# Performance work log

Measured on AMD Instinct MI355X. Metric: run time of the kernel, lower is better.

Reference implementation:

```python
import jax, jax.numpy as jnp
import numpy as np

B, CIN, COUT = 16, 64, 64
H, W = 96, 96
HK, AK = 3, 3  # hidden_kernels, attn_kernels


def setup_inputs() -> dict:
    key = jax.random.key(0)
    k1, k2, k3, k4, k5 = jax.random.split(key, 5)
    s = 1.0 / np.sqrt(CIN * HK * HK)
    return {
        "x1": jax.random.normal(k1, (B, CIN, H, W), jnp.float32),
        "x2": jax.random.normal(k2, (B, CIN, H, W), jnp.float32),
        "w1": jax.random.normal(k3, (COUT, CIN, HK, HK), jnp.float32) * s,
        "w2": jax.random.normal(k4, (COUT, CIN, HK, HK), jnp.float32) * s,
        "w3": jax.random.normal(k5, (COUT, CIN, HK, HK), jnp.float32) * s,
    }


def _conv(x, w):
    p = HK // 2
    return jax.lax.conv_general_dilated(x, w, (1, 1), [(p, p), (p, p)])


def _unfold_strided(x):
    # nn.Unfold(AK, stride=AK): non-overlapping AK x AK patches.
    # [B,C,H,W] -> [B, C*AK*AK, (H//AK)*(W//AK)], channel order (C, kh, kw).
    b, c, h, w = x.shape
    hp, wp = h // AK, w // AK
    x = x.reshape(b, c, hp, AK, wp, AK).transpose(0, 1, 3, 5, 2, 4)
    return x.reshape(b, c * AK * AK, hp * wp)


def _unfold_padded(x):
    # nn.Unfold(AK, padding=AK//2): stride-1 patches, output length H*W (AK odd).
    b, c, h, w = x.shape
    p = AK // 2
    xp = jnp.pad(x, ((0, 0), (0, 0), (p, p), (p, p)))
    cols = [xp[:, :, i:i + h, j:j + w] for i in range(AK) for j in range(AK)]
    return jnp.stack(cols, axis=2).reshape(b, c * AK * AK, h * w)


def reference(x1, x2, w1, w2, w3):
    aa = AK * AK
    L = (H // AK) * (W // AK)
    kf = _conv(x1, w1)   # [B, Cout, H, W]
    qf = _conv(x2, w2)
    vf = _conv(x1, w3)
    # key: [B, aa, Cout, L]; query: [B, aa, L, Cout]
    key = _unfold_strided(kf).reshape(B, COUT, aa, L).transpose(0, 2, 1, 3)
    qry = _unfold_strided(qf).reshape(B, COUT, aa, L).transpose(0, 2, 3, 1)
    # scores[b,k,c,d] over patches -> [B, aa, Cout_k, Cout_q]
    scores = jnp.einsum('bkcl,bkld->bkcd', key, qry)
    # transpose(1,3).flatten(2): [B, Cout_q, Cout_k*aa]
    scores = scores.transpose(0, 3, 2, 1).reshape(B, COUT, COUT * aa)
    scores = scores / np.sqrt(COUT * aa).astype(np.float32)
    attn = jax.nn.softmax(scores, axis=2)  # dynamic conv kernels
    vcols = _unfold_padded(vf)             # [B, Cout*aa, H*W]
    out = jnp.einsum('bce,bel->bcl', attn, vcols)
    return out.reshape(B, COUT, H, W)
```

## Files before the change

### kernel.cpp

```cpp
#include <hip/hip_runtime.h>


typedef __attribute__((ext_vector_type(8))) short short8v;
typedef __attribute__((ext_vector_type(4))) float floatx4;
typedef __attribute__((ext_vector_type(4))) unsigned int uint4v;

constexpr int PLANE = 9216;
constexpr int SCP_STRIDE = 589824;

__device__ __forceinline__ unsigned short f2bf(float f) {
    unsigned int u = __float_as_uint(f);
    u = (u + 0x7FFFu + ((u >> 16) & 1u)) >> 16;
    return (unsigned short)u;
}

__global__ __launch_bounds__(256) void nchw2nhwc_bf16(
    const float* __restrict__ x, unsigned short* __restrict__ xh)
{
    int blk = blockIdx.x;
    int b = blk / 96, y = blk - b * 96;
    __shared__ float ls[64][96];
    const float* xp = x + (size_t)b * 64 * PLANE + (size_t)y * 96;
    for (int i = threadIdx.x; i < 64 * 96; i += 256) {
        int ci = i / 96, xc = i - ci * 96;
        ls[ci][xc] = xp[(size_t)ci * PLANE + xc];
    }
    __syncthreads();
    unsigned short* op = xh + ((size_t)b * PLANE + (size_t)y * 96) * 64;
    for (int i = threadIdx.x; i < 96 * 8; i += 256) {
        int xc = i >> 3, cg = i & 7;
        unsigned short tmp[8] __attribute__((aligned(16)));
        #pragma unroll
        for (int j = 0; j < 8; ++j) tmp[j] = f2bf(ls[cg * 8 + j][xc]);
        *(uint4v*)&op[(size_t)xc * 64 + cg * 8] = *(const uint4v*)tmp;
    }
}

__global__ __launch_bounds__(256) void wreorder(
    const float* __restrict__ w1, const float* __restrict__ w2,
    const float* __restrict__ w3, unsigned short* __restrict__ wl)
{
    int blk = blockIdx.x;
    int wi = blk / 9, k9 = blk - wi * 9;
    const float* w = (wi == 0) ? w1 : ((wi == 1) ? w2 : w3);
    unsigned short* o = wl + (size_t)wi * 9 * 4096 + (size_t)k9 * 4096;
    for (int i = threadIdx.x; i < 4096; i += 256)
        o[i] = f2bf(w[(size_t)i * 9 + k9]);
}

__global__ __launch_bounds__(256) void conv_mfma(
    const unsigned short* __restrict__ xh,
    const unsigned short* __restrict__ wl,
    void* __restrict__ out, int omode, int dynb)
{
    int blk = blockIdx.x;
    int xs3 = blk % 3; int t = blk / 3;
    int yq = t % 12;   int b = t / 12;
    int x0 = xs3 * 32, y0 = yq * 8;

    __shared__ __align__(16) unsigned short xs[10 * 34 * 64];

    const unsigned short* xb = xh + (size_t)b * PLANE * 64;
    for (int i = threadIdx.x; i < 2720; i += 256) {
        int g = i & 7, pix = i >> 3;
        int pr = pix / 34, pc = pix - pr * 34;
        int y = y0 - 1 + pr, x = x0 - 1 + pc;
        uint4v v = {0u, 0u, 0u, 0u};
        if ((unsigned)y < 96u && (unsigned)x < 96u)
            v = *(const uint4v*)&xb[((size_t)y * 96 + x) * 64 + g * 8];
        *(uint4v*)&xs[pix * 64 + (g ^ (pc & 7)) * 8] = v;
    }
    __syncthreads();

    int lane = threadIdx.x & 63;
    int w = threadIdx.x >> 6;
    int ln = lane & 15, quad = lane >> 4;
    int coh  = (w & 1) * 32;
    int rowh = (w >> 1) * 4;

    const unsigned short* wb = wl + (dynb ? (size_t)b * 9 * 4096 : 0);

    floatx4 acc[2][8];
    #pragma unroll
    for (int mi = 0; mi < 2; ++mi)
        #pragma unroll
        for (int nt = 0; nt < 8; ++nt) acc[mi][nt] = (floatx4){0.f, 0.f, 0.f, 0.f};

    #pragma unroll
    for (int k9 = 0; k9 < 9; ++k9) {
        int dy = k9 / 3, dx = k9 - dy * 3;
        #pragma unroll
        for (int ch = 0; ch < 2; ++ch) {
            short8v a0 = *(const short8v*)
                &wb[((size_t)k9 * 64 + coh + ln) * 64 + ch * 32 + quad * 8];
            short8v a1 = *(const short8v*)
                &wb[((size_t)k9 * 64 + coh + 16 + ln) * 64 + ch * 32 + quad * 8];
            int gb = ch * 4 + quad;
            #pragma unroll
            for (int nt = 0; nt < 8; ++nt) {
                int n = nt * 16 + ln;
                int r = rowh + (n >> 5) + dy;
                int c = (n & 31) + dx;
                short8v bf = *(const short8v*)
                    &xs[(r * 34 + c) * 64 + (gb ^ (c & 7)) * 8];
                acc[0][nt] = __builtin_amdgcn_mfma_f32_16x16x32_bf16(a0, bf, acc[0][nt], 0, 0, 0);
                acc[1][nt] = __builtin_amdgcn_mfma_f32_16x16x32_bf16(a1, bf, acc[1][nt], 0, 0, 0);
            }
        }
    }

    #pragma unroll
    for (int nt = 0; nt < 8; ++nt) {
        int n = nt * 16 + ln;
        int y = y0 + rowh + (n >> 5), x = x0 + (n & 31);
        if (omode == 2) {
            float* o = (float*)out;
            #pragma unroll
            for (int mi = 0; mi < 2; ++mi)
                #pragma unroll
                for (int reg = 0; reg < 4; ++reg) {
                    int co = coh + mi * 16 + quad * 4 + reg;
                    o[((size_t)(b * 64 + co)) * PLANE + (size_t)y * 96 + x] = acc[mi][nt][reg];
                }
        } else if (omode == 1) {
            unsigned short* o = (unsigned short*)out;
            #pragma unroll
            for (int mi = 0; mi < 2; ++mi) {
                unsigned short tmp[4] __attribute__((aligned(8)));
                #pragma unroll
                for (int reg = 0; reg < 4; ++reg) tmp[reg] = f2bf(acc[mi][nt][reg]);
                *(uint2*)&o[((size_t)b * PLANE + (size_t)y * 96 + x) * 64 + coh + mi * 16 + quad * 4]
                    = *(const uint2*)tmp;
            }
        } else {
            unsigned short* o = (unsigned short*)out;
            int k9 = (y % 3) * 3 + (x % 3);
            int l = (y / 3) * 32 + (x / 3);
            #pragma unroll
            for (int mi = 0; mi < 2; ++mi)
                #pragma unroll
                for (int reg = 0; reg < 4; ++reg) {
                    int co = coh + mi * 16 + quad * 4 + reg;
                    o[((size_t)(b * 9 + k9) * 64 + co) * 1024 + l] = f2bf(acc[mi][nt][reg]);
                }
        }
    }
}

__global__ __launch_bounds__(256) void scores_mfma(
    const unsigned short* __restrict__ kfc, const unsigned short* __restrict__ qfc,
    float* __restrict__ scp, int nseg)
{
    int blk = blockIdx.x;
    int seg = blk % nseg;
    int bk  = blk / nseg;
    int lane = threadIdx.x & 63, w = threadIdx.x >> 6;
    int ln = lane & 15, quad = lane >> 4;
    const unsigned short* ka = kfc + (size_t)bk * 64 * 1024;
    const unsigned short* qa = qfc + (size_t)bk * 64 * 1024;

    int Kblk = 1024 / nseg;
    int Kw   = Kblk / 4;
    int nch  = Kw / 32;

    floatx4 acc[4][4];
    #pragma unroll
    for (int i = 0; i < 4; ++i)
        #pragma unroll
        for (int j = 0; j < 4; ++j) acc[i][j] = (floatx4){0.f, 0.f, 0.f, 0.f};

    for (int chk = 0; chk < nch; ++chk) {
        int l = seg * Kblk + w * Kw + chk * 32 + quad * 8;
        short8v a[4], bq[4];
        #pragma unroll
        for (int mi = 0; mi < 4; ++mi)
            a[mi] = *(const short8v*)&ka[(size_t)(mi * 16 + ln) * 1024 + l];
        #pragma unroll
        for (int ni = 0; ni < 4; ++ni)
            bq[ni] = *(const short8v*)&qa[(size_t)(ni * 16 + ln) * 1024 + l];
        #pragma unroll
        for (int mi = 0; mi < 4; ++mi)
            #pragma unroll
            for (int ni = 0; ni < 4; ++ni)
                acc[mi][ni] = __builtin_amdgcn_mfma_f32_16x16x32_bf16(a[mi], bq[ni], acc[mi][ni], 0, 0, 0);
    }

    __shared__ float ls[4][64][65];
    #pragma unroll
    for (int mi = 0; mi < 4; ++mi)
        #pragma unroll
        for (int ni = 0; ni < 4; ++ni)
            #pragma unroll
            for (int reg = 0; reg < 4; ++reg)
                ls[w][ni * 16 + ln][mi * 16 + quad * 4 + reg] = acc[mi][ni][reg];
    __syncthreads();

    float* op = scp + (size_t)seg * SCP_STRIDE + (size_t)bk * 4096;
    int t = threadIdx.x;
    #pragma unroll
    for (int j = 0; j < 16; ++j) {
        int e = t * 16 + j;
        int d = e >> 6, c = e & 63;
        op[e] = ls[0][d][c] + ls[1][d][c] + ls[2][d][c] + ls[3][d][c];
    }
}

__global__ __launch_bounds__(256) void softmax_kernel(
    const float* __restrict__ scp, unsigned short* __restrict__ dynw, int nseg)
{
    int w = threadIdx.x >> 6, c = threadIdx.x & 63;
    int row = blockIdx.x * 4 + w;
    int b = row >> 6, d = row & 63;
    float v[9];
    float mx = -3.0e38f;
    #pragma unroll
    for (int k = 0; k < 9; ++k) {
        size_t idx = (size_t)(b * 9 + k) * 4096 + d * 64 + c;
        float s = scp[idx];
        for (int g = 1; g < nseg; ++g) s += scp[(size_t)g * SCP_STRIDE + idx];
        v[k] = s * (1.0f / 24.0f);
        mx = fmaxf(mx, v[k]);
    }
    #pragma unroll
    for (int o = 32; o; o >>= 1) mx = fmaxf(mx, __shfl_xor(mx, o));
    float sum = 0.f;
    #pragma unroll
    for (int k = 0; k < 9; ++k) { v[k] = __expf(v[k] - mx); sum += v[k]; }
    #pragma unroll
    for (int o = 32; o; o >>= 1) sum += __shfl_xor(sum, o);
    float inv = 1.0f / sum;
    #pragma unroll
    for (int k = 0; k < 9; ++k)
        dynw[((size_t)(b * 9 + k) * 64 + d) * 64 + c] = f2bf(v[k] * inv);
}

extern "C" void kernel_launch(void* const* d_in, const int* in_sizes, int n_in,
                              void* d_out, int out_size, void* d_ws, size_t ws_size,
                              hipStream_t stream) {
    (void)in_sizes; (void)n_in; (void)out_size;
    const float* x1 = (const float*)d_in[0];
    const float* x2 = (const float*)d_in[1];
    const float* w1 = (const float*)d_in[2];
    const float* w2 = (const float*)d_in[3];
    const float* w3 = (const float*)d_in[4];
    float* out = (float*)d_out;

    char* ws = (char*)d_ws;
    constexpr size_t XHB = (size_t)16 * PLANE * 64 * 2;
    unsigned short* xh1 = (unsigned short*)(ws);
    unsigned short* xh2 = (unsigned short*)(ws + XHB);
    unsigned short* kfc = (unsigned short*)(ws + 2 * XHB);
    unsigned short* qfc = (unsigned short*)(ws + 3 * XHB);
    unsigned short* wl  = (unsigned short*)(ws + 4 * XHB);
    unsigned short* dynw = (unsigned short*)(ws + 4 * XHB + 221184);
    float* scp = (float*)(ws + 4 * XHB + 221184 + 1179648);

    size_t base = 4 * XHB + 221184 + 1179648;
    int nseg = (ws_size >= base + 2 * (size_t)SCP_STRIDE * 4) ? 2 : 1;

    nchw2nhwc_bf16<<<dim3(1536), dim3(256), 0, stream>>>(x1, xh1);
    nchw2nhwc_bf16<<<dim3(1536), dim3(256), 0, stream>>>(x2, xh2);
    wreorder<<<dim3(27), dim3(256), 0, stream>>>(w1, w2, w3, wl);

    conv_mfma<<<dim3(576), dim3(256), 0, stream>>>(xh1, wl,            kfc, 3, 0);
    conv_mfma<<<dim3(576), dim3(256), 0, stream>>>(xh2, wl + 9 * 4096, qfc, 3, 0);
    scores_mfma<<<dim3(144 * nseg), dim3(256), 0, stream>>>(kfc, qfc, scp, nseg);
    softmax_kernel<<<dim3(256), dim3(256), 0, stream>>>(scp, dynw, nseg);
    conv_mfma<<<dim3(576), dim3(256), 0, stream>>>(xh1, wl + 18 * 4096, xh2, 1, 0);
    conv_mfma<<<dim3(576), dim3(256), 0, stream>>>(xh2, dynw, out, 2, 1);
}
```

Before: 286.9 us.

## Batch the three convolutions into one launch and retile conv per wave row

Merges the two NCHW->NHWC conversions into one launch. Fuses the k, q and v convolutions into a single conv_mfma grid of 3456 blocks, which writes v to a separate workspace buffer when the workspace is large enough. The conv tile shrinks from 8 rows to 4: each wave now owns one image row and computes all 64 output channels, loading 4 weight fragments and 2 input fragments per step. Launch bounds are raised for occupancy. This cuts launch count and tail effects, and the v convolution can now overlap with the k and q work, at the cost of more weight fragment loads per block and extra halo reloads.

```diff
diff --git a/kernel.cpp b/kernel.cpp
--- a/kernel.cpp
+++ b/kernel.cpp
@@ -15,9 +15,13 @@
 }
 
 __global__ __launch_bounds__(256) void nchw2nhwc_bf16(
-    const float* __restrict__ x, unsigned short* __restrict__ xh)
+    const float* __restrict__ x1, unsigned short* __restrict__ xh1,
+    const float* __restrict__ x2, unsigned short* __restrict__ xh2)
 {
     int blk = blockIdx.x;
+    const float* x = (blk < 1536) ? x1 : x2;
+    unsigned short* xh = (blk < 1536) ? xh1 : xh2;
+    if (blk >= 1536) blk -= 1536;
     int b = blk / 96, y = blk - b * 96;
     __shared__ float ls[64][96];
     const float* xp = x + (size_t)b * 64 * PLANE + (size_t)y * 96;
@@ -48,20 +52,29 @@
         o[i] = f2bf(w[(size_t)i * 9 + k9]);
 }
 
-__global__ __launch_bounds__(256) void conv_mfma(
-    const unsigned short* __restrict__ xh,
+__global__ __launch_bounds__(256, 4) void conv_mfma(
+    const unsigned short* __restrict__ in0,
+    const unsigned short* __restrict__ in1,
+    const unsigned short* __restrict__ in2,
     const unsigned short* __restrict__ wl,
-    void* __restrict__ out, int omode, int dynb)
+    void* __restrict__ o0, void* __restrict__ o1, void* __restrict__ o2,
+    int om0, int om1, int om2, int dynb)
 {
     int blk = blockIdx.x;
-    int xs3 = blk % 3; int t = blk / 3;
-    int yq = t % 12;   int b = t / 12;
-    int x0 = xs3 * 32, y0 = yq * 8;
-
-    __shared__ __align__(16) unsigned short xs[10 * 34 * 64];
-
-    const unsigned short* xb = xh + (size_t)b * PLANE * 64;
-    for (int i = threadIdx.x; i < 2720; i += 256) {
+    int cid = blk / 1152;
+    int r0  = blk - cid * 1152;
+    int xs3 = r0 % 3; int t = r0 / 3;
+    int yq = t % 24;  int b = t / 24;
+    int x0 = xs3 * 32, y0 = yq * 4;
+
+    const unsigned short* xin = (cid == 0) ? in0 : (cid == 1) ? in1 : in2;
+    void* out  = (cid == 0) ? o0 : (cid == 1) ? o1 : o2;
+    int omode  = (cid == 0) ? om0 : (cid == 1) ? om1 : om2;
+
+    __shared__ __align__(16) unsigned short xs[6 * 34 * 64];
+
+    const unsigned short* xb = xin + (size_t)b * PLANE * 64;
+    for (int i = threadIdx.x; i < 1632; i += 256) {
         int g = i & 7, pix = i >> 3;
         int pr = pix / 34, pc = pix - pr * 34;
         int y = y0 - 1 + pr, x = x0 - 1 + pc;
@@ -75,61 +88,64 @@
     int lane = threadIdx.x & 63;
     int w = threadIdx.x >> 6;
     int ln = lane & 15, quad = lane >> 4;
-    int coh  = (w & 1) * 32;
-    int rowh = (w >> 1) * 4;
-
-    const unsigned short* wb = wl + (dynb ? (size_t)b * 9 * 4096 : 0);
-
-    floatx4 acc[2][8];
-    #pragma unroll
-    for (int mi = 0; mi < 2; ++mi)
-        #pragma unroll
-        for (int nt = 0; nt < 8; ++nt) acc[mi][nt] = (floatx4){0.f, 0.f, 0.f, 0.f};
+
+    const unsigned short* wb = wl + (dynb ? (size_t)b * 9 * 4096
+                                          : (size_t)cid * 9 * 4096);
+
+    floatx4 acc[4][2];
+    #pragma unroll
+    for (int m = 0; m < 4; ++m)
+        #pragma unroll
+        for (int nh = 0; nh < 2; ++nh) acc[m][nh] = (floatx4){0.f, 0.f, 0.f, 0.f};
 
     #pragma unroll
     for (int k9 = 0; k9 < 9; ++k9) {
         int dy = k9 / 3, dx = k9 - dy * 3;
         #pragma unroll
         for (int ch = 0; ch < 2; ++ch) {
-            short8v a0 = *(const short8v*)
-                &wb[((size_t)k9 * 64 + coh + ln) * 64 + ch * 32 + quad * 8];
-            short8v a1 = *(const short8v*)
-                &wb[((size_t)k9 * 64 + coh + 16 + ln) * 64 + ch * 32 + quad * 8];
+            short8v a[4];
+            #pragma unroll
+            for (int m = 0; m < 4; ++m)
+                a[m] = *(const short8v*)
+                    &wb[((size_t)k9 * 64 + m * 16 + ln) * 64 + ch * 32 + quad * 8];
             int gb = ch * 4 + quad;
-            #pragma unroll
-            for (int nt = 0; nt < 8; ++nt) {
-                int n = nt * 16 + ln;
-                int r = rowh + (n >> 5) + dy;
-                int c = (n & 31) + dx;
-                short8v bf = *(const short8v*)
-                    &xs[(r * 34 + c) * 64 + (gb ^ (c & 7)) * 8];
-                acc[0][nt] = __builtin_amdgcn_mfma_f32_16x16x32_bf16(a0, bf, acc[0][nt], 0, 0, 0);
-                acc[1][nt] = __builtin_amdgcn_mfma_f32_16x16x32_bf16(a1, bf, acc[1][nt], 0, 0, 0);
+            short8v bf[2];
+            #pragma unroll
+            for (int nh = 0; nh < 2; ++nh) {
+                int c = nh * 16 + ln + dx;
+                int r = w + dy;
+                bf[nh] = *(const short8v*)&xs[(r * 34 + c) * 64 + (gb ^ (c & 7)) * 8];
             }
+            #pragma unroll
+            for (int m = 0; m < 4; ++m)
+                #pragma unroll
+                for (int nh = 0; nh < 2; ++nh)
+                    acc[m][nh] = __builtin_amdgcn_mfma_f32_16x16x32_bf16(
+                        a[m], bf[nh], acc[m][nh], 0, 0, 0);
         }
     }
 
-    #pragma unroll
-    for (int nt = 0; nt < 8; ++nt) {
-        int n = nt * 16 + ln;
-        int y = y0 + rowh + (n >> 5), x = x0 + (n & 31);
+    int y = y0 + w;
+    #pragma unroll
+    for (int nh = 0; nh < 2; ++nh) {
+        int x = x0 + nh * 16 + ln;
         if (omode == 2) {
             float* o = (float*)out;
             #pragma unroll
-            for (int mi = 0; mi < 2; ++mi)
+            for (int m = 0; m < 4; ++m)
                 #pragma unroll
                 for (int reg = 0; reg < 4; ++reg) {
-                    int co = coh + mi * 16 + quad * 4 + reg;
-                    o[((size_t)(b * 64 + co)) * PLANE + (size_t)y * 96 + x] = acc[mi][nt][reg];
+                    int co = m * 16 + quad * 4 + reg;
+                    o[((size_t)(b * 64 + co)) * PLANE + (size_t)y * 96 + x] = acc[m][nh][reg];
                 }
         } else if (omode == 1) {
             unsigned short* o = (unsigned short*)out;
             #pragma unroll
-            for (int mi = 0; mi < 2; ++mi) {
+            for (int m = 0; m < 4; ++m) {
                 unsigned short tmp[4] __attribute__((aligned(8)));
                 #pragma unroll
-                for (int reg = 0; reg < 4; ++reg) tmp[reg] = f2bf(acc[mi][nt][reg]);
-                *(uint2*)&o[((size_t)b * PLANE + (size_t)y * 96 + x) * 64 + coh + mi * 16 + quad * 4]
+                for (int reg = 0; reg < 4; ++reg) tmp[reg] = f2bf(acc[m][nh][reg]);
+                *(uint2*)&o[((size_t)b * PLANE + (size_t)y * 96 + x) * 64 + m * 16 + quad * 4]
                     = *(const uint2*)tmp;
             }
         } else {
@@ -137,11 +153,11 @@
             int k9 = (y % 3) * 3 + (x % 3);
             int l = (y / 3) * 32 + (x / 3);
             #pragma unroll
-            for (int mi = 0; mi < 2; ++mi)
+            for (int m = 0; m < 4; ++m)
                 #pragma unroll
                 for (int reg = 0; reg < 4; ++reg) {
-                    int co = coh + mi * 16 + quad * 4 + reg;
-                    o[((size_t)(b * 9 + k9) * 64 + co) * 1024 + l] = f2bf(acc[mi][nt][reg]);
+                    int co = m * 16 + quad * 4 + reg;
+                    o[((size_t)(b * 9 + k9) * 64 + co) * 1024 + l] = f2bf(acc[m][nh][reg]);
                 }
         }
     }
@@ -182,7 +198,8 @@
         for (int mi = 0; mi < 4; ++mi)
             #pragma unroll
             for (int ni = 0; ni < 4; ++ni)
-                acc[mi][ni] = __builtin_amdgcn_mfma_f32_16x16x32_bf16(a[mi], bq[ni], acc[mi][ni], 0, 0, 0);
+                acc[mi][ni] = __builtin_amdgcn_mfma_f32_16x16x32_bf16(
+                    a[mi], bq[ni], acc[mi][ni], 0, 0, 0);
     }
 
     __shared__ float ls[4][64][65];
@@ -247,25 +264,43 @@
 
     char* ws = (char*)d_ws;
     constexpr size_t XHB = (size_t)16 * PLANE * 64 * 2;
-    unsigned short* xh1 = (unsigned short*)(ws);
-    unsigned short* xh2 = (unsigned short*)(ws + XHB);
-    unsigned short* kfc = (unsigned short*)(ws + 2 * XHB);
-    unsigned short* qfc = (unsigned short*)(ws + 3 * XHB);
-    unsigned short* wl  = (unsigned short*)(ws + 4 * XHB);
-    unsigned short* dynw = (unsigned short*)(ws + 4 * XHB + 221184);
-    float* scp = (float*)(ws + 4 * XHB + 221184 + 1179648);
-
-    size_t base = 4 * XHB + 221184 + 1179648;
-    int nseg = (ws_size >= base + 2 * (size_t)SCP_STRIDE * 4) ? 2 : 1;
-
-    nchw2nhwc_bf16<<<dim3(1536), dim3(256), 0, stream>>>(x1, xh1);
-    nchw2nhwc_bf16<<<dim3(1536), dim3(256), 0, stream>>>(x2, xh2);
+    constexpr size_t WLB = 221184;
+    constexpr size_t DWB = 1179648;
+    constexpr size_t SCB = (size_t)SCP_STRIDE * 4;
+
+    unsigned short* xh1  = (unsigned short*)(ws);
+    unsigned short* xh2  = (unsigned short*)(ws + XHB);
+    unsigned short* kfc  = (unsigned short*)(ws + 2 * XHB);
+    unsigned short* qfc  = (unsigned short*)(ws + 3 * XHB);
+    unsigned short* wl   = (unsigned short*)(ws + 4 * XHB);
+    unsigned short* dynw = (unsigned short*)(ws + 4 * XHB + WLB);
+    float* scp = (float*)(ws + 4 * XHB + WLB + DWB);
+    size_t base = 4 * XHB + WLB + DWB;
+
+    int nseg; bool fused3;
+    if (ws_size >= base + 2 * SCB + XHB)      { nseg = 2; fused3 = true; }
+    else if (ws_size >= base + 1 * SCB + XHB) { nseg = 1; fused3 = true; }
+    else { nseg = (ws_size >= base + 2 * SCB) ? 2 : 1; fused3 = false; }
+    unsigned short* vf = (unsigned short*)(ws + base + (size_t)nseg * SCB);
+
+    nchw2nhwc_bf16<<<dim3(3072), dim3(256), 0, stream>>>(x1, xh1, x2, xh2);
     wreorder<<<dim3(27), dim3(256), 0, stream>>>(w1, w2, w3, wl);
 
-    conv_mfma<<<dim3(576), dim3(256), 0, stream>>>(xh1, wl,            kfc, 3, 0);
-    conv_mfma<<<dim3(576), dim3(256), 0, stream>>>(xh2, wl + 9 * 4096, qfc, 3, 0);
-    scores_mfma<<<dim3(144 * nseg), dim3(256), 0, stream>>>(kfc, qfc, scp, nseg);
-    softmax_kernel<<<dim3(256), dim3(256), 0, stream>>>(scp, dynw, nseg);
-    conv_mfma<<<dim3(576), dim3(256), 0, stream>>>(xh1, wl + 18 * 4096, xh2, 1, 0);
-    conv_mfma<<<dim3(576), dim3(256), 0, stream>>>(xh2, dynw, out, 2, 1);
-}
+    if (fused3) {
+        conv_mfma<<<dim3(3456), dim3(256), 0, stream>>>(
+            xh1, xh2, xh1, wl, kfc, qfc, vf, 3, 3, 1, 0);
+        scores_mfma<<<dim3(144 * nseg), dim3(256), 0, stream>>>(kfc, qfc, scp, nseg);
+        softmax_kernel<<<dim3(256), dim3(256), 0, stream>>>(scp, dynw, nseg);
+        conv_mfma<<<dim3(1152), dim3(256), 0, stream>>>(
+            vf, nullptr, nullptr, dynw, out, nullptr, nullptr, 2, 0, 0, 1);
+    } else {
+        conv_mfma<<<dim3(2304), dim3(256), 0, stream>>>(
+            xh1, xh2, nullptr, wl, kfc, qfc, nullptr, 3, 3, 0, 0);
+        scores_mfma<<<dim3(144 * nseg), dim3(256), 0, stream>>>(kfc, qfc, scp, nseg);
+        softmax_kernel<<<dim3(256), dim3(256), 0, stream>>>(scp, dynw, nseg);
+        conv_mfma<<<dim3(1152), dim3(256), 0, stream>>>(
+            xh1, nullptr, nullptr, wl + 18 * 4096, xh2, nullptr, nullptr, 1, 0, 0, 0);
+        conv_mfma<<<dim3(1152), dim3(256), 0, stream>>>(
+            xh2, nullptr, nullptr, dynw, out, nullptr, nullptr, 2, 0, 0, 1);
+    }
+}
```

Result: slower. 350.6 us (+22.2%).
